# Performance work log

Measured on AMD Instinct MI355X. Metric: run time of the kernel, lower is better.

The kernel has to match this reference:

```python
import jax, jax.numpy as jnp
import numpy as np

KS = 4     # kernel_size
PAD = 2    # padding
M = 4      # number of value branches
OC = 64    # out_channels
IC = 3     # in_channels


def _patches(t, H, W):
    # t: (..., Hp, Wp) -> (..., H, W, KS*KS); stride=1 local windows,
    # flattened as i*KS + j to match torch unfold(2).unfold(3) + view(-1).
    cols = [t[..., i:i + H, j:j + W] for i in range(KS) for j in range(KS)]
    return jnp.stack(cols, axis=-1)


def setup_inputs() -> dict:
    key = jax.random.key(0)
    ks = jax.random.split(key, 7)
    B, H, W = 4, 128, 128
    x = jax.random.normal(ks[0], (B, IC, H, W), dtype=jnp.float32)
    # kaiming fan_out for 1x1 convs: std = sqrt(2 / fan_out) = sqrt(2/OC)
    std = np.sqrt(2.0 / OC).astype(np.float32)
    key_w = jax.random.normal(ks[1], (OC, IC), dtype=jnp.float32) * std
    query_w = jax.random.normal(ks[2], (OC, IC), dtype=jnp.float32) * std
    value_w = jax.random.normal(ks[3], (M, OC, IC), dtype=jnp.float32) * std
    emb_a = jax.random.normal(ks[4], (OC, KS), dtype=jnp.float32)
    emb_b = jax.random.normal(ks[5], (OC, KS), dtype=jnp.float32)
    emb_mix = jax.random.normal(ks[6], (M, OC), dtype=jnp.float32)
    return {"x": x, "key_w": key_w, "query_w": query_w, "value_w": value_w,
            "emb_a": emb_a, "emb_b": emb_b, "emb_mix": emb_mix}


def reference(x, key_w, query_w, value_w, emb_a, emb_b, emb_mix):
    B, C, H, W = x.shape
    xp = jnp.pad(x, ((0, 0), (0, 0), (PAD, PAD), (PAD, PAD)))
    # 1x1 convs as channel contractions
    q = jnp.einsum('oi,bihw->bohw', query_w, x)            # (B,OC,H,W)
    k = jnp.einsum('oi,bihw->bohw', key_w, xp)             # (B,OC,Hp,Wp)
    v = jnp.einsum('moi,bihw->mbohw', value_w, xp)         # (M,B,OC,Hp,Wp)
    kp = _patches(k, H, W)                                 # (B,OC,H,W,KS*KS)
    vp = _patches(v, H, W)                                 # (M,B,OC,H,W,KS*KS)
    # relative-position mixing logits, softmax over the m axis
    la = emb_mix @ emb_a                                   # (M,KS)
    lb = emb_mix @ emb_b                                   # (M,KS)
    emb = la[:, :, None] + lb[:, None, :]                  # (M,KS,KS)
    emb = jax.nn.softmax(emb.reshape(M, KS * KS), axis=0)  # (M,KS*KS)
    vsum = jnp.einsum('mk,mbohwk->bohwk', emb, vp)         # sum over m branches
    # groups=1: per-pixel local softmax over the KS*KS window
    attn = jax.nn.softmax(q[..., None] * kp, axis=-1)
    out = jnp.einsum('bohwk,bohwk->bohw', attn, vsum)      # (B,OC,H,W)
    return out
```

## Files before the change

### kernel.cpp

```cpp
#include <hip/hip_runtime.h>
#include <math.h>

#define B_  4
#define IC_ 3
#define OC_ 64
#define M_  4
#define KS_ 4
#define PAD_ 2
#define H_  128
#define W_  128
#define KK_ 16

#if __has_builtin(__builtin_amdgcn_exp2f)
#define EXP2(x) __builtin_amdgcn_exp2f(x)
#else
#define EXP2(x) __expf((x) * 0.69314718055994531f)
#endif

__global__ __launch_bounds__(64) void attn_prep_kernel(
    const float* __restrict__ key_w,
    const float* __restrict__ query_w,
    const float* __restrict__ value_w,
    const float* __restrict__ emb_a,
    const float* __restrict__ emb_b,
    const float* __restrict__ emb_mix,
    float* __restrict__ wtab)
{
    __shared__ float s_embm[M_][KK_];
    const int tid = threadIdx.x;

    if (tid < KK_) {
        const int i = tid >> 2;
        const int j = tid & 3;
        float l[M_];
        #pragma unroll
        for (int m = 0; m < M_; ++m) {
            float la = 0.f, lb = 0.f;
            for (int c = 0; c < OC_; ++c) {
                const float emc = emb_mix[m * OC_ + c];
                la = fmaf(emc, emb_a[c * KS_ + i], la);
                lb = fmaf(emc, emb_b[c * KS_ + j], lb);
            }
            l[m] = la + lb;
        }
        float mx = fmaxf(fmaxf(l[0], l[1]), fmaxf(l[2], l[3]));
        float e0 = __expf(l[0] - mx);
        float e1 = __expf(l[1] - mx);
        float e2 = __expf(l[2] - mx);
        float e3 = __expf(l[3] - mx);
        const float inv = 1.f / (e0 + e1 + e2 + e3);
        s_embm[0][tid] = e0 * inv;
        s_embm[1][tid] = e1 * inv;
        s_embm[2][tid] = e2 * inv;
        s_embm[3][tid] = e3 * inv;
    }
    __syncthreads();

    const int o = tid;
    float* rec = wtab + o * 64;
    rec[0] = query_w[o * 3 + 0];
    rec[1] = query_w[o * 3 + 1];
    rec[2] = query_w[o * 3 + 2];
    rec[3] = key_w[o * 3 + 0];
    rec[4] = key_w[o * 3 + 1];
    rec[5] = key_w[o * 3 + 2];
    rec[6] = 0.f;
    rec[7] = 0.f;
    #pragma unroll
    for (int k = 0; k < KK_; ++k) {
        #pragma unroll
        for (int c = 0; c < IC_; ++c) {
            float acc = 0.f;
            #pragma unroll
            for (int m = 0; m < M_; ++m)
                acc = fmaf(s_embm[m][k], value_w[(m * OC_ + o) * IC_ + c], acc);
            rec[8 + k * 3 + c] = acc;
        }
    }
}

__global__ __launch_bounds__(256) void attn_main_kernel(
    const float* __restrict__ x,
    const float* __restrict__ wtab,
    float* __restrict__ out)
{
    const int tid = threadIdx.x;
    const int bi  = blockIdx.x;
    const int wt  = bi & 1;
    const int oh  = (bi >> 1) & 1;
    const int h   = (bi >> 2) & (H_ - 1);
    const int b   = bi >> 9;
    const int w   = wt * 64 + (tid & 63);
    const int ob  = __builtin_amdgcn_readfirstlane(oh * 32 + (tid >> 6) * 8);

    float p[IC_][KK_];
    #pragma unroll
    for (int c = 0; c < IC_; ++c) {
        const float* __restrict__ xc = x + (((b * IC_ + c) << 7) << 7);
        #pragma unroll
        for (int i = 0; i < KS_; ++i) {
            const int hy = h + i - PAD_;
            const bool rok = (unsigned)hy < (unsigned)H_;
            #pragma unroll
            for (int j = 0; j < KS_; ++j) {
                const int wx = w + j - PAD_;
                const bool ok = rok && ((unsigned)wx < (unsigned)W_);
                p[c][i * KS_ + j] = ok ? xc[(hy << 7) + wx] : 0.f;
            }
        }
    }

    const float* __restrict__ recbase = wtab + ob * 64;
    #pragma unroll
    for (int oo = 0; oo < 8; ++oo) {
        const float* __restrict__ rec = recbase + oo * 64;
        const float qw0 = rec[0], qw1 = rec[1], qw2 = rec[2];
        const float kw0 = rec[3], kw1 = rec[4], kw2 = rec[5];
        const float q  = fmaf(qw0, p[0][10], fmaf(qw1, p[1][10], qw2 * p[2][10]));
        const float qs = q * 1.4426950408889634f;
        float num = 0.f, den = 0.f;
        #pragma unroll
        for (int k = 0; k < KK_; ++k) {
            const float kd = fmaf(kw0, p[0][k], fmaf(kw1, p[1][k], kw2 * p[2][k]));
            const float vs = fmaf(rec[8 + k * 3 + 0], p[0][k],
                             fmaf(rec[8 + k * 3 + 1], p[1][k],
                                  rec[8 + k * 3 + 2] * p[2][k]));
            const float e = EXP2(qs * kd);
            num = fmaf(e, vs, num);
            den += e;
        }
        const int o = ob + oo;
        out[((b * OC_ + o) << 14) + (h << 7) + w] = num * __builtin_amdgcn_rcpf(den);
    }
}

extern "C" void kernel_launch(void* const* d_in, const int* in_sizes, int n_in,
                              void* d_out, int out_size, void* d_ws, size_t ws_size,
                              hipStream_t stream) {
    const float* x       = (const float*)d_in[0];
    const float* key_w   = (const float*)d_in[1];
    const float* query_w = (const float*)d_in[2];
    const float* value_w = (const float*)d_in[3];
    const float* emb_a   = (const float*)d_in[4];
    const float* emb_b   = (const float*)d_in[5];
    const float* emb_mix = (const float*)d_in[6];
    float* wtab = (float*)d_ws;
    float* out  = (float*)d_out;

    attn_prep_kernel<<<1, 64, 0, stream>>>(key_w, query_w, value_w,
                                           emb_a, emb_b, emb_mix, wtab);
    const int grid = B_ * H_ * 2 * 2;
    attn_main_kernel<<<grid, 256, 0, stream>>>(x, wtab, out);
}
```

Measured before the change: 101.1 us.

## Pre-pad input into workspace and use vector loads plus scalar constant weights

The prep kernel now also writes a zero-padded copy of x into the workspace, which lets the main kernel drop its per-tap bounds checks and load each 4-wide window row with one unaligned 16-byte load. Weight records are read through the constant address space so the compiler can use scalar loads. The query scale is folded into the key weights to save a multiply per tap. The cost is an extra pass that writes and rereads the padded input, plus a larger prep launch.

```diff
diff --git a/kernel.cpp b/kernel.cpp
--- a/kernel.cpp
+++ b/kernel.cpp
@@ -1,5 +1,6 @@
 #include <hip/hip_runtime.h>
 #include <math.h>
+#include <stdint.h>
 
 #define B_  4
 #define IC_ 3
@@ -10,6 +11,12 @@
 #define H_  128
 #define W_  128
 #define KK_ 16
+#define PH_ 132
+#define PW_ 132
+#define PPLANE_ (PH_ * PW_)
+#define NPAD_   (B_ * IC_ * PPLANE_)
+#define NPADBLK_ ((NPAD_ + 255) / 256)
+#define WTAB_FLOATS_ 4096
 
 #if __has_builtin(__builtin_amdgcn_exp2f)
 #define EXP2(x) __builtin_amdgcn_exp2f(x)
@@ -17,18 +24,41 @@
 #define EXP2(x) __expf((x) * 0.69314718055994531f)
 #endif
 
-__global__ __launch_bounds__(64) void attn_prep_kernel(
+struct __attribute__((packed, aligned(4))) F4 { float x0, x1, x2, x3; };
+
+typedef const __attribute__((address_space(4))) float cfloat;
+
+__global__ __launch_bounds__(256) void attn_prep_kernel(
+    const float* __restrict__ x,
     const float* __restrict__ key_w,
     const float* __restrict__ query_w,
     const float* __restrict__ value_w,
     const float* __restrict__ emb_a,
     const float* __restrict__ emb_b,
     const float* __restrict__ emb_mix,
-    float* __restrict__ wtab)
+    float* __restrict__ wtab,
+    float* __restrict__ xpad)
 {
-    __shared__ float s_embm[M_][KK_];
     const int tid = threadIdx.x;
 
+    if (blockIdx.x < NPADBLK_) {
+        const int idx = blockIdx.x * 256 + tid;
+        if (idx < NPAD_) {
+            const int plane = idx / PPLANE_;
+            const int r     = idx - plane * PPLANE_;
+            const int hy    = r / PW_;
+            const int wx    = r - hy * PW_;
+            const int hs = hy - PAD_;
+            const int ws = wx - PAD_;
+            float v = 0.f;
+            if ((unsigned)hs < (unsigned)H_ && (unsigned)ws < (unsigned)W_)
+                v = x[(plane << 14) + (hs << 7) + ws];
+            xpad[idx] = v;
+        }
+        return;
+    }
+
+    __shared__ float s_embm[M_][KK_];
     if (tid < KK_) {
         const int i = tid >> 2;
         const int j = tid & 3;
@@ -56,31 +86,33 @@
     }
     __syncthreads();
 
-    const int o = tid;
-    float* rec = wtab + o * 64;
-    rec[0] = query_w[o * 3 + 0];
-    rec[1] = query_w[o * 3 + 1];
-    rec[2] = query_w[o * 3 + 2];
-    rec[3] = key_w[o * 3 + 0];
-    rec[4] = key_w[o * 3 + 1];
-    rec[5] = key_w[o * 3 + 2];
-    rec[6] = 0.f;
-    rec[7] = 0.f;
-    #pragma unroll
-    for (int k = 0; k < KK_; ++k) {
+    if (tid < OC_) {
+        const int o = tid;
+        float* rec = wtab + o * 64;
+        rec[0] = query_w[o * 3 + 0];
+        rec[1] = query_w[o * 3 + 1];
+        rec[2] = query_w[o * 3 + 2];
+        rec[3] = key_w[o * 3 + 0];
+        rec[4] = key_w[o * 3 + 1];
+        rec[5] = key_w[o * 3 + 2];
+        rec[6] = 0.f;
+        rec[7] = 0.f;
         #pragma unroll
-        for (int c = 0; c < IC_; ++c) {
-            float acc = 0.f;
+        for (int k = 0; k < KK_; ++k) {
             #pragma unroll
-            for (int m = 0; m < M_; ++m)
-                acc = fmaf(s_embm[m][k], value_w[(m * OC_ + o) * IC_ + c], acc);
-            rec[8 + k * 3 + c] = acc;
+            for (int c = 0; c < IC_; ++c) {
+                float acc = 0.f;
+                #pragma unroll
+                for (int m = 0; m < M_; ++m)
+                    acc = fmaf(s_embm[m][k], value_w[(m * OC_ + o) * IC_ + c], acc);
+                rec[8 + k * 3 + c] = acc;
+            }
         }
     }
 }
 
 __global__ __launch_bounds__(256) void attn_main_kernel(
-    const float* __restrict__ x,
+    const float* __restrict__ xpad,
     const float* __restrict__ wtab,
     float* __restrict__ out)
 {
@@ -96,41 +128,40 @@
     float p[IC_][KK_];
     #pragma unroll
     for (int c = 0; c < IC_; ++c) {
-        const float* __restrict__ xc = x + (((b * IC_ + c) << 7) << 7);
+        const float* rowp = xpad + (b * IC_ + c) * PPLANE_ + h * PW_ + w;
         #pragma unroll
         for (int i = 0; i < KS_; ++i) {
-            const int hy = h + i - PAD_;
-            const bool rok = (unsigned)hy < (unsigned)H_;
-            #pragma unroll
-            for (int j = 0; j < KS_; ++j) {
-                const int wx = w + j - PAD_;
-                const bool ok = rok && ((unsigned)wx < (unsigned)W_);
-                p[c][i * KS_ + j] = ok ? xc[(hy << 7) + wx] : 0.f;
-            }
+            const F4 v = *(const F4*)(rowp + i * PW_);
+            p[c][i * 4 + 0] = v.x0;
+            p[c][i * 4 + 1] = v.x1;
+            p[c][i * 4 + 2] = v.x2;
+            p[c][i * 4 + 3] = v.x3;
         }
     }
 
-    const float* __restrict__ recbase = wtab + ob * 64;
+    cfloat* crec0 = (cfloat*)(uintptr_t)(wtab + ob * 64);
+
     #pragma unroll
     for (int oo = 0; oo < 8; ++oo) {
-        const float* __restrict__ rec = recbase + oo * 64;
-        const float qw0 = rec[0], qw1 = rec[1], qw2 = rec[2];
-        const float kw0 = rec[3], kw1 = rec[4], kw2 = rec[5];
-        const float q  = fmaf(qw0, p[0][10], fmaf(qw1, p[1][10], qw2 * p[2][10]));
+        cfloat* rec = crec0 + oo * 64;
+        const float q  = fmaf(rec[0], p[0][10], fmaf(rec[1], p[1][10], rec[2] * p[2][10]));
         const float qs = q * 1.4426950408889634f;
+        const float kws0 = rec[3] * qs;
+        const float kws1 = rec[4] * qs;
+        const float kws2 = rec[5] * qs;
         float num = 0.f, den = 0.f;
         #pragma unroll
         for (int k = 0; k < KK_; ++k) {
-            const float kd = fmaf(kw0, p[0][k], fmaf(kw1, p[1][k], kw2 * p[2][k]));
-            const float vs = fmaf(rec[8 + k * 3 + 0], p[0][k],
-                             fmaf(rec[8 + k * 3 + 1], p[1][k],
-                                  rec[8 + k * 3 + 2] * p[2][k]));
-            const float e = EXP2(qs * kd);
+            const float a0 = p[0][k], a1 = p[1][k], a2 = p[2][k];
+            const float t  = fmaf(kws0, a0, fmaf(kws1, a1, kws2 * a2));
+            const float e  = EXP2(t);
+            const float vs = fmaf(rec[8 + k*3 + 0], a0,
+                              fmaf(rec[8 + k*3 + 1], a1,
+                                   rec[8 + k*3 + 2] * a2));
             num = fmaf(e, vs, num);
             den += e;
         }
-        const int o = ob + oo;
-        out[((b * OC_ + o) << 14) + (h << 7) + w] = num * __builtin_amdgcn_rcpf(den);
+        out[((b * OC_ + ob + oo) << 14) + (h << 7) + w] = num * __builtin_amdgcn_rcpf(den);
     }
 }
 
@@ -145,10 +176,10 @@
     const float* emb_b   = (const float*)d_in[5];
     const float* emb_mix = (const float*)d_in[6];
     float* wtab = (float*)d_ws;
+    float* xpad = (float*)d_ws + WTAB_FLOATS_;
     float* out  = (float*)d_out;
 
-    attn_prep_kernel<<<1, 64, 0, stream>>>(key_w, query_w, value_w,
-                                           emb_a, emb_b, emb_mix, wtab);
-    const int grid = B_ * H_ * 2 * 2;
-    attn_main_kernel<<<grid, 256, 0, stream>>>(x, wtab, out);
+    attn_prep_kernel<<<NPADBLK_ + 1, 256, 0, stream>>>(
+        x, key_w, query_w, value_w, emb_a, emb_b, emb_mix, wtab, xpad);
+    attn_main_kernel<<<B_ * H_ * 2 * 2, 256, 0, stream>>>(xpad, wtab, out);
 }
```

Result: faster. 97.35 us (-3.7%).
